# Performance work log

Measured on AMD Instinct MI355X. Metric: run time of the kernel, lower is better.

## Reference

```python
import jax, jax.numpy as jnp
import numpy as np
from jax import lax

A, T, B, OBS, H, ACT = 4, 128, 256, 128, 128, 8  # agents, time, envs, obs_dim, gru_hidden(=embed), act_dim


def setup_inputs() -> dict:
    key = jax.random.key(0)
    ks = jax.random.split(key, 16)
    def w(k, shape, fan_in):
        return (jax.random.normal(k, shape, jnp.float32) / np.float32(np.sqrt(fan_in)))
    return {
        "hstate": jnp.zeros((A, B, H), jnp.float32),
        "obs": jax.random.normal(ks[0], (A, T, B, OBS), jnp.float32),
        "avail_actions": jnp.ones((A, T, B, ACT), jnp.float32),
        # embedding dense
        "We": w(ks[1], (A, OBS, H), OBS), "be": jnp.zeros((A, H), jnp.float32),
        # GRU: input kernels (r|z|n concat) with bias, hidden kernels (r|z|n), only n-hidden has bias
        "Wi": w(ks[2], (A, H, 3 * H), H), "bi": jnp.zeros((A, 3 * H), jnp.float32),
        "Wh": w(ks[3], (A, H, 3 * H), H), "bhn": jnp.zeros((A, H), jnp.float32),
        # actor head
        "Wa1": w(ks[4], (A, H, H), H), "ba1": jnp.zeros((A, H), jnp.float32),
        "Wa2": 0.01 * w(ks[5], (A, H, ACT), H), "ba2": jnp.zeros((A, ACT), jnp.float32),
        "log_std": jnp.zeros((A, ACT), jnp.float32),
        # critic head
        "Wc1": w(ks[6], (A, H, H), H), "bc1": jnp.zeros((A, H), jnp.float32),
        "Wc2": w(ks[7], (A, H, 1), H), "bc2": jnp.zeros((A, 1), jnp.float32),
        "done": jax.random.bernoulli(ks[8], 0.05, (A, T, B)),
    }


def _agent_forward(h0, obs, done, avail_actions, We, be, Wi, bi, Wh, bhn,
                   Wa1, ba1, Wa2, ba2, log_std, Wc1, bc1, Wc2, bc2):
    # obs: [T,B,OBS], done: [T,B], h0: [B,H]
    act = jnp.tanh  # config['network']['activation'] == 'tanh'
    emb = act(jnp.einsum('tbo,oh->tbh', obs, We) + be)          # [T,B,H]
    xi = jnp.einsum('tbh,hg->tbg', emb, Wi) + bi                # [T,B,3H] precomputed input gates

    def step(h, xs):
        xi_t, d = xs                                            # [B,3H], [B]
        h = jnp.where(d[:, None], 0.0, h)                       # reset on done
        hh = h @ Wh                                             # [B,3H]
        xr, xz, xn = jnp.split(xi_t, 3, axis=-1)
        hr, hz, hn = jnp.split(hh, 3, axis=-1)
        r = jax.nn.sigmoid(xr + hr)
        z = jax.nn.sigmoid(xz + hz)
        n = jnp.tanh(xn + r * (hn + bhn))
        h_new = (1.0 - z) * n + z * h
        return h_new, h_new

    hT, ys = lax.scan(step, h0, (xi, done))                     # ys: [T,B,H]
    a = act(jnp.einsum('tbh,hk->tbk', ys, Wa1) + ba1)
    mean = jnp.einsum('tbh,ha->tba', a, Wa2) + ba2              # [T,B,ACT]
    std = jnp.exp(log_std)                                      # [ACT]
    c = act(jnp.einsum('tbh,hk->tbk', ys, Wc1) + bc1)
    value = (jnp.einsum('tbh,ho->tbo', c, Wc2) + bc2)[..., 0]   # [T,B]
    return hT, mean, std, value


def reference(hstate, obs, avail_actions, We, be, Wi, bi, Wh, bhn,
              Wa1, ba1, Wa2, ba2, log_std, Wc1, bc1, Wc2, bc2, done):
    hT, mean, std, value = jax.vmap(_agent_forward)(
        hstate, obs, done, avail_actions, We, be, Wi, bi, Wh, bhn,
        Wa1, ba1, Wa2, ba2, log_std, Wc1, bc1, Wc2, bc2)
    return hT, mean, std, value
```

## Files before the change

kernel.cpp:

```cpp
#include <hip/hip_runtime.h>

typedef unsigned short u16;
typedef __attribute__((ext_vector_type(8))) short short8;
typedef __attribute__((ext_vector_type(4))) float f32x4;

#define A_ 4
#define T_ 128
#define B_ 256
#define OBS_ 128
#define H_ 128
#define G_ 384
#define ACT_ 8

__device__ __forceinline__ u16 f2b(float x) {
    unsigned int u = __float_as_uint(x);
    u = (u + 0x7fffu + ((u >> 16) & 1u)) >> 16;
    return (u16)u;
}
__device__ __forceinline__ u16 f2bc(float x) {
    return (u16)((__float_as_uint(x) + 0x8000u) >> 16);
}
__device__ __forceinline__ float b2f(u16 h) {
    return __uint_as_float(((unsigned int)h) << 16);
}
__device__ __forceinline__ float fexp2_(float x) { return __builtin_amdgcn_exp2f(x); }
__device__ __forceinline__ float frcp_(float x) { return __builtin_amdgcn_rcpf(x); }
__device__ __forceinline__ float sigmoidf_(float x) {
    return frcp_(1.0f + fexp2_(-1.4426950408889634f * x));
}
__device__ __forceinline__ float tanhf_(float x) {
    return 1.0f - 2.0f * frcp_(1.0f + fexp2_(2.8853900817779268f * x));
}
__device__ __forceinline__ f32x4 mfma16(short8 a, short8 b, f32x4 c) {
    return __builtin_amdgcn_mfma_f32_16x16x32_bf16(a, b, c, 0, 0, 0);
}
__device__ __forceinline__ void barrier_fast() {
    asm volatile("s_waitcnt lgkmcnt(0)\n\ts_barrier" ::: "memory");
}

__global__ void k_prep(const float* __restrict__ We, const float* __restrict__ Wi,
                       const float* __restrict__ Wh, const float* __restrict__ Wa1,
                       const float* __restrict__ Wc1, const float* __restrict__ Wa2,
                       const float* __restrict__ Wc2, const float* __restrict__ log_std,
                       u16* __restrict__ weT, u16* __restrict__ wiT, u16* __restrict__ whT,
                       u16* __restrict__ wa1T, u16* __restrict__ wc1T, u16* __restrict__ h2T,
                       float* __restrict__ std_out) {
    const int PER_A = 149504;
    int idx = blockIdx.x * 256 + threadIdx.x;
    const int total = 4 * PER_A;
    if (idx < total) {
        int a = idx / PER_A;
        int i = idx % PER_A;
        if (i < 16384) {
            int h = i >> 7, o = i & 127;
            weT[a * 16384 + i] = f2b(We[a * 16384 + o * 128 + h]);
        } else if (i < 16384 + 49152) {
            int j = i - 16384; int g = j >> 7, k = j & 127;
            wiT[a * 49152 + j] = f2b(Wi[a * 49152 + k * 384 + g]);
        } else if (i < 16384 + 2 * 49152) {
            int j = i - 16384 - 49152; int g = j >> 7, k = j & 127;
            whT[a * 49152 + j] = f2b(Wh[a * 49152 + k * 384 + g]);
        } else if (i < 2 * 16384 + 2 * 49152) {
            int j = i - 16384 - 2 * 49152; int h2 = j >> 7, k = j & 127;
            wa1T[a * 16384 + j] = f2b(Wa1[a * 16384 + k * 128 + h2]);
        } else if (i < 3 * 16384 + 2 * 49152) {
            int j = i - 2 * 16384 - 2 * 49152; int h2 = j >> 7, k = j & 127;
            wc1T[a * 16384 + j] = f2b(Wc1[a * 16384 + k * 128 + h2]);
        } else {
            int j = i - 3 * 16384 - 2 * 49152; int row = j >> 7, k = j & 127;
            float v = 0.f;
            if (row < 8) v = Wa2[a * 1024 + k * 8 + row];
            else if (row == 8) v = Wc2[a * 128 + k];
            h2T[a * 2048 + j] = f2b(v);
        }
    } else if (idx < total + 32) {
        int i = idx - total;
        std_out[i] = __expf(log_std[i]);
    }
}

__global__ __launch_bounds__(512, 2) void k_embed_xi(
    const float* __restrict__ obs, const float* __restrict__ be, const float* __restrict__ bi,
    const u16* __restrict__ weT, const u16* __restrict__ wiT, u16* __restrict__ xi_ws) {
    __shared__ __align__(16) u16 obsl[16][136];
    __shared__ __align__(16) u16 elds[16][136];
    const int a = blockIdx.y, t = blockIdx.x;
    const int wid = threadIdx.x >> 6, lane = threadIdx.x & 63;
    const int m = lane & 15, quad = lane >> 4;
    const int srow = threadIdx.x >> 5, schunk = threadIdx.x & 31;

    short8 we[4], wi[3][4];
    {
        const u16* p = weT + a * 16384 + (wid * 16 + m) * 128 + quad * 8;
#pragma unroll
        for (int ks = 0; ks < 4; ++ks) we[ks] = *(const short8*)(p + ks * 32);
#pragma unroll
        for (int g = 0; g < 3; ++g) {
            const u16* q = wiT + a * 49152 + (g * 128 + wid * 16 + m) * 128 + quad * 8;
#pragma unroll
            for (int ks = 0; ks < 4; ++ks) wi[g][ks] = *(const short8*)(q + ks * 32);
        }
    }
    const float bee = be[a * H_ + wid * 16 + m];
    float big[3];
#pragma unroll
    for (int g = 0; g < 3; ++g) big[g] = bi[a * G_ + g * 128 + wid * 16 + m];

    const float* obsrow = obs + ((size_t)(a * T_ + t) * B_ + srow) * OBS_ + schunk * 4;
    float4 pf = *(const float4*)(obsrow);
    ushort4* xi4 = (ushort4*)xi_ws;

    for (int it = 0; it < 16; ++it) {
        ushort4 ob;
        ob.x = f2b(pf.x); ob.y = f2b(pf.y); ob.z = f2b(pf.z); ob.w = f2b(pf.w);
        *(ushort4*)&obsl[srow][schunk * 4] = ob;
        barrier_fast();
        if (it + 1 < 16) pf = *(const float4*)(obsrow + (size_t)(it + 1) * 2048);

        short8 af[4];
#pragma unroll
        for (int ks = 0; ks < 4; ++ks)
            af[ks] = *(const short8*)&obsl[m][ks * 32 + quad * 8];
        f32x4 acc = f32x4{0.f, 0.f, 0.f, 0.f};
#pragma unroll
        for (int ks = 0; ks < 4; ++ks) acc = mfma16(af[ks], we[ks], acc);
#pragma unroll
        for (int r = 0; r < 4; ++r)
            elds[quad * 4 + r][wid * 16 + m] = f2b(tanhf_(acc[r] + bee));
        barrier_fast();

        short8 ef[4];
#pragma unroll
        for (int ks = 0; ks < 4; ++ks)
            ef[ks] = *(const short8*)&elds[m][ks * 32 + quad * 8];
        f32x4 xa[3];
#pragma unroll
        for (int g = 0; g < 3; ++g) xa[g] = f32x4{0.f, 0.f, 0.f, 0.f};
#pragma unroll
        for (int ks = 0; ks < 4; ++ks)
#pragma unroll
            for (int g = 0; g < 3; ++g) xa[g] = mfma16(ef[ks], wi[g][ks], xa[g]);

        const size_t base = ((size_t)(a * 16 + it) * T_ + t) * 1536;
#pragma unroll
        for (int g = 0; g < 3; ++g) {
            ushort4 pk;
            pk.x = f2b(xa[g][0] + big[g]);
            pk.y = f2b(xa[g][1] + big[g]);
            pk.z = f2b(xa[g][2] + big[g]);
            pk.w = f2b(xa[g][3] + big[g]);
            xi4[base + (size_t)(wid * 3 + g) * 64 + lane] = pk;
        }
    }
}

__global__ __launch_bounds__(512, 2) void k_scan(
    const float* __restrict__ hstate, const u16* __restrict__ xi_ws,
    const u16* __restrict__ whT, const float* __restrict__ bhn,
    const int* __restrict__ done, u16* __restrict__ ys_ws, float* __restrict__ hT_out) {
    __shared__ __align__(16) u16 hlds[2][16][136];
    const int a = blockIdx.y, btile = blockIdx.x;
    const int wid = threadIdx.x >> 6, lane = threadIdx.x & 63;
    const int m = lane & 15, quad = lane >> 4;
    const int b0 = btile * 16;
    const int col = 16 * wid + m;

    short8 wh[3][4];
    const u16* whTa = whT + a * 49152;
#pragma unroll
    for (int g = 0; g < 3; ++g) {
        const u16* p = whTa + (g * 128 + col) * 128 + quad * 8;
#pragma unroll
        for (int ks = 0; ks < 4; ++ks) wh[g][ks] = *(const short8*)(p + ks * 32);
    }

    float hm[4]; u16 hb[4];
#pragma unroll
    for (int r = 0; r < 4; ++r) {
        float v = hstate[((size_t)a * B_ + b0 + quad * 4 + r) * H_ + col];
        hm[r] = v; hb[r] = f2b(v);
    }
    const float bh = bhn[a * H_ + col];

    const ushort4* xi4 = (const ushort4*)xi_ws;
    const size_t xibase = ((size_t)(a * 16 + btile) * T_) * 1536 + wid * 192 + lane;
    const int* dptr = done + (size_t)a * T_ * B_ + b0 + quad * 4;

    ushort4 pA0 = xi4[xibase], pA1 = xi4[xibase + 64], pA2 = xi4[xibase + 128];
    ushort4 pB0 = xi4[xibase + 1536], pB1 = xi4[xibase + 1536 + 64], pB2 = xi4[xibase + 1536 + 128];
    int4 dA = *(const int4*)(dptr);
    int4 dB = *(const int4*)(dptr + B_);

#define SCAN_STEP(t, P0, P1, P2, DN, BUF)                                           \
    {                                                                               \
        u16(*hl)[136] = hlds[BUF];                                                  \
        if (DN.x) { hm[0] = 0.f; hb[0] = 0; }                                       \
        if (DN.y) { hm[1] = 0.f; hb[1] = 0; }                                       \
        if (DN.z) { hm[2] = 0.f; hb[2] = 0; }                                       \
        if (DN.w) { hm[3] = 0.f; hb[3] = 0; }                                       \
        hl[quad * 4 + 0][col] = hb[0];                                              \
        hl[quad * 4 + 1][col] = hb[1];                                              \
        hl[quad * 4 + 2][col] = hb[2];                                              \
        hl[quad * 4 + 3][col] = hb[3];                                              \
        barrier_fast();                                                             \
        float xr[4], xz[4], xn[4];                                                  \
        xr[0] = b2f(P0.x); xr[1] = b2f(P0.y); xr[2] = b2f(P0.z); xr[3] = b2f(P0.w); \
        xz[0] = b2f(P1.x); xz[1] = b2f(P1.y); xz[2] = b2f(P1.z); xz[3] = b2f(P1.w); \
        xn[0] = b2f(P2.x); xn[1] = b2f(P2.y); xn[2] = b2f(P2.z); xn[3] = b2f(P2.w); \
        if ((t) + 2 < T_) {                                                         \
            const size_t nx = xibase + (size_t)((t) + 2) * 1536;                    \
            P0 = xi4[nx]; P1 = xi4[nx + 64]; P2 = xi4[nx + 128];                    \
            DN = *(const int4*)(dptr + (size_t)((t) + 2) * B_);                     \
        }                                                                           \
        short8 af[4];                                                               \
        af[0] = *(const short8*)&hl[m][0 * 32 + quad * 8];                          \
        af[1] = *(const short8*)&hl[m][1 * 32 + quad * 8];                          \
        af[2] = *(const short8*)&hl[m][2 * 32 + quad * 8];                          \
        af[3] = *(const short8*)&hl[m][3 * 32 + quad * 8];                          \
        f32x4 ar = f32x4{0.f, 0.f, 0.f, 0.f};                                       \
        f32x4 az = f32x4{0.f, 0.f, 0.f, 0.f};                                       \
        f32x4 an = f32x4{0.f, 0.f, 0.f, 0.f};                                       \
        _Pragma("unroll") for (int ks = 0; ks < 4; ++ks) {                          \
            ar = mfma16(af[ks], wh[0][ks], ar);                                     \
            az = mfma16(af[ks], wh[1][ks], az);                                     \
            an = mfma16(af[ks], wh[2][ks], an);                                     \
        }                                                                           \
        u16* yp = ys_ws + (((size_t)a * T_ + (t)) * B_ + b0 + quad * 4) * H_ + col; \
        _Pragma("unroll") for (int r = 0; r < 4; ++r) {                             \
            const float rg = sigmoidf_(xr[r] + ar[r]);                              \
            const float zg = sigmoidf_(xz[r] + az[r]);                              \
            const float ng = tanhf_(fmaf(rg, an[r] + bh, xn[r]));                   \
            const float hn2 = fmaf(zg, hm[r] - ng, ng);                             \
            hm[r] = hn2;                                                            \
            hb[r] = f2bc(hn2);                                                      \
            yp[(size_t)r * H_] = hb[r];                                             \
        }                                                                           \
    }

    for (int t = 0; t < T_; t += 2) {
        SCAN_STEP(t, pA0, pA1, pA2, dA, 0);
        SCAN_STEP(t + 1, pB0, pB1, pB2, dB, 1);
    }
#undef SCAN_STEP

#pragma unroll
    for (int r = 0; r < 4; ++r)
        hT_out[((size_t)a * B_ + b0 + quad * 4 + r) * H_ + col] = hm[r];
}

__global__ __launch_bounds__(512, 2) void k_heads(
    const u16* __restrict__ ys_ws, const u16* __restrict__ wa1T, const u16* __restrict__ wc1T,
    const u16* __restrict__ h2T, const float* __restrict__ ba1, const float* __restrict__ bc1,
    const float* __restrict__ ba2, const float* __restrict__ bc2,
    float* __restrict__ mean_out, float* __restrict__ val_out) {
    __shared__ __align__(16) u16 ysl[16][136];
    __shared__ __align__(16) u16 al[2][16][136];
    const int a = blockIdx.y;
    const int wid = threadIdx.x >> 6, lane = threadIdx.x & 63;
    const int m = lane & 15, quad = lane >> 4;
    const int srow = threadIdx.x >> 5, schunk = threadIdx.x & 31;

    short8 wa[4], wc[4], h2f[4];
    {
        const u16* pa = wa1T + a * 16384 + (wid * 16 + m) * 128 + quad * 8;
        const u16* pc = wc1T + a * 16384 + (wid * 16 + m) * 128 + quad * 8;
        const u16* ph = h2T + a * 2048 + m * 128 + quad * 8;
#pragma unroll
        for (int ks = 0; ks < 4; ++ks) {
            wa[ks] = *(const short8*)(pa + ks * 32);
            wc[ks] = *(const short8*)(pc + ks * 32);
            h2f[ks] = *(const short8*)(ph + ks * 32);
        }
    }
    const float fa = ba1[a * 128 + wid * 16 + m];
    const float fc = bc1[a * 128 + wid * 16 + m];

    const u16* ysbase = ys_ws + ((size_t)a * 32768 + (size_t)blockIdx.x * 256 + srow) * 128 + schunk * 4;
    ushort4 pf = *(const ushort4*)(ysbase);

    for (int it = 0; it < 16; ++it) {
        *(ushort4*)&ysl[srow][schunk * 4] = pf;
        barrier_fast();
        if (it + 1 < 16) pf = *(const ushort4*)(ysbase + (size_t)(it + 1) * 2048);

        short8 yf[4];
#pragma unroll
        for (int ks = 0; ks < 4; ++ks)
            yf[ks] = *(const short8*)&ysl[m][ks * 32 + quad * 8];
        f32x4 aa = f32x4{0.f, 0.f, 0.f, 0.f};
        f32x4 ac = f32x4{0.f, 0.f, 0.f, 0.f};
#pragma unroll
        for (int ks = 0; ks < 4; ++ks) {
            aa = mfma16(yf[ks], wa[ks], aa);
            ac = mfma16(yf[ks], wc[ks], ac);
        }
#pragma unroll
        for (int r = 0; r < 4; ++r) {
            al[0][quad * 4 + r][wid * 16 + m] = f2b(tanhf_(aa[r] + fa));
            al[1][quad * 4 + r][wid * 16 + m] = f2b(tanhf_(ac[r] + fc));
        }
        barrier_fast();

        if (wid < 2) {
            short8 tf[4];
#pragma unroll
            for (int ks = 0; ks < 4; ++ks)
                tf[ks] = *(const short8*)&al[wid][m][ks * 32 + quad * 8];
            f32x4 tacc = f32x4{0.f, 0.f, 0.f, 0.f};
#pragma unroll
            for (int ks = 0; ks < 4; ++ks) tacc = mfma16(tf[ks], h2f[ks], tacc);
            const size_t R0 = (size_t)a * 32768 + (size_t)(blockIdx.x * 16 + it) * 16;
            if (wid == 0) {
                if (m < 8) {
                    const float bb = ba2[a * 8 + m];
#pragma unroll
                    for (int r = 0; r < 4; ++r)
                        mean_out[(R0 + quad * 4 + r) * 8 + m] = tacc[r] + bb;
                }
            } else {
                if (m == 8) {
                    const float bb = bc2[a];
#pragma unroll
                    for (int r = 0; r < 4; ++r)
                        val_out[R0 + quad * 4 + r] = tacc[r] + bb;
                }
            }
        }
    }
}

extern "C" void kernel_launch(void* const* d_in, const int* in_sizes, int n_in,
                              void* d_out, int out_size, void* d_ws, size_t ws_size,
                              hipStream_t stream) {
    const float* hstate = (const float*)d_in[0];
    const float* obs = (const float*)d_in[1];
    const float* We = (const float*)d_in[3];
    const float* be = (const float*)d_in[4];
    const float* Wi = (const float*)d_in[5];
    const float* bi = (const float*)d_in[6];
    const float* Wh = (const float*)d_in[7];
    const float* bhn = (const float*)d_in[8];
    const float* Wa1 = (const float*)d_in[9];
    const float* ba1 = (const float*)d_in[10];
    const float* Wa2 = (const float*)d_in[11];
    const float* ba2 = (const float*)d_in[12];
    const float* log_std = (const float*)d_in[13];
    const float* Wc1 = (const float*)d_in[14];
    const float* bc1 = (const float*)d_in[15];
    const float* Wc2 = (const float*)d_in[16];
    const float* bc2 = (const float*)d_in[17];
    const int* done = (const int*)d_in[18];

    float* out = (float*)d_out;
    float* hT_out = out;
    float* mean_out = out + 131072;
    float* std_out = out + 1179648;
    float* val_out = out + 1179680;

    u16* ws = (u16*)d_ws;
    u16* xi = ws;
    u16* ys = xi + 50331648;
    u16* weT = ys + 16777216;
    u16* wiT = weT + 65536;
    u16* whT = wiT + 196608;
    u16* wa1T = whT + 196608;
    u16* wc1T = wa1T + 65536;
    u16* h2T = wc1T + 65536;

    hipLaunchKernelGGL(k_prep, dim3(2337), dim3(256), 0, stream,
                       We, Wi, Wh, Wa1, Wc1, Wa2, Wc2, log_std,
                       weT, wiT, whT, wa1T, wc1T, h2T, std_out);
    hipLaunchKernelGGL(k_embed_xi, dim3(128, 4), dim3(512), 0, stream,
                       obs, be, bi, weT, wiT, xi);
    hipLaunchKernelGGL(k_scan, dim3(16, 4), dim3(512), 0, stream,
                       hstate, xi, whT, bhn, done, ys, hT_out);
    hipLaunchKernelGGL(k_heads, dim3(128, 4), dim3(512), 0, stream,
                       ys, wa1T, wc1T, h2T, ba1, bc1, ba2, bc2, mean_out, val_out);
}
```

Before: 312.2 us.

## Pack two batch tiles per scan block and strength-reduce scan pointers

The GRU scan kernel now runs 1024-thread blocks, each covering two 16-row batch tiles, so the grid is half as many blocks, each with its own pair of LDS hidden-state buffers. Per-step address computation for the xi, done and ys streams becomes pointer increments instead of recomputed offsets. Launch bounds are raised on both the scan and heads kernels to request higher occupancy. The risks are that each step's barrier now spans sixteen waves, and that the tighter launch bounds may force register spills in the weight-resident scan and head kernels.

```diff
diff --git a/kernel.cpp b/kernel.cpp
--- a/kernel.cpp
+++ b/kernel.cpp
@@ -154,16 +154,19 @@
     }
 }
 
-__global__ __launch_bounds__(512, 2) void k_scan(
+__global__ __launch_bounds__(1024, 4) void k_scan(
     const float* __restrict__ hstate, const u16* __restrict__ xi_ws,
     const u16* __restrict__ whT, const float* __restrict__ bhn,
     const int* __restrict__ done, u16* __restrict__ ys_ws, float* __restrict__ hT_out) {
-    __shared__ __align__(16) u16 hlds[2][16][136];
-    const int a = blockIdx.y, btile = blockIdx.x;
+    __shared__ __align__(16) u16 hlds[2][2][16][136];
+    const int a = blockIdx.y;
     const int wid = threadIdx.x >> 6, lane = threadIdx.x & 63;
+    const int bl = wid >> 3;
+    const int wq = wid & 7;
+    const int btile = blockIdx.x * 2 + bl;
     const int m = lane & 15, quad = lane >> 4;
     const int b0 = btile * 16;
-    const int col = 16 * wid + m;
+    const int col = 16 * wq + m;
 
     short8 wh[3][4];
     const u16* whTa = whT + a * 49152;
@@ -183,7 +186,7 @@
     const float bh = bhn[a * H_ + col];
 
     const ushort4* xi4 = (const ushort4*)xi_ws;
-    const size_t xibase = ((size_t)(a * 16 + btile) * T_) * 1536 + wid * 192 + lane;
+    const size_t xibase = ((size_t)(a * 16 + btile) * T_) * 1536 + wq * 192 + lane;
     const int* dptr = done + (size_t)a * T_ * B_ + b0 + quad * 4;
 
     ushort4 pA0 = xi4[xibase], pA1 = xi4[xibase + 64], pA2 = xi4[xibase + 128];
@@ -191,9 +194,16 @@
     int4 dA = *(const int4*)(dptr);
     int4 dB = *(const int4*)(dptr + B_);
 
-#define SCAN_STEP(t, P0, P1, P2, DN, BUF)                                           \
+    const ushort4* xpA = xi4 + xibase + 2 * 1536;
+    const ushort4* xpB = xi4 + xibase + 3 * 1536;
+    const int* dpA = dptr + 2 * B_;
+    const int* dpB = dptr + 3 * B_;
+    u16* ypA = ys_ws + ((size_t)a * T_ * B_ + b0 + quad * 4) * H_ + col;
+    u16* ypB = ypA + (size_t)B_ * H_;
+
+#define SCAN_STEP(t, P0, P1, P2, DN, XP, DP, YP, BUF)                               \
     {                                                                               \
-        u16(*hl)[136] = hlds[BUF];                                                  \
+        u16(*hl)[136] = hlds[bl][BUF];                                              \
         if (DN.x) { hm[0] = 0.f; hb[0] = 0; }                                       \
         if (DN.y) { hm[1] = 0.f; hb[1] = 0; }                                       \
         if (DN.z) { hm[2] = 0.f; hb[2] = 0; }                                       \
@@ -208,10 +218,10 @@
         xz[0] = b2f(P1.x); xz[1] = b2f(P1.y); xz[2] = b2f(P1.z); xz[3] = b2f(P1.w); \
         xn[0] = b2f(P2.x); xn[1] = b2f(P2.y); xn[2] = b2f(P2.z); xn[3] = b2f(P2.w); \
         if ((t) + 2 < T_) {                                                         \
-            const size_t nx = xibase + (size_t)((t) + 2) * 1536;                    \
-            P0 = xi4[nx]; P1 = xi4[nx + 64]; P2 = xi4[nx + 128];                    \
-            DN = *(const int4*)(dptr + (size_t)((t) + 2) * B_);                     \
+            P0 = XP[0]; P1 = XP[64]; P2 = XP[128];                                  \
+            DN = *(const int4*)(DP);                                                \
         }                                                                           \
+        XP += 3072; DP += 2 * B_;                                                   \
         short8 af[4];                                                               \
         af[0] = *(const short8*)&hl[m][0 * 32 + quad * 8];                          \
         af[1] = *(const short8*)&hl[m][1 * 32 + quad * 8];                          \
@@ -225,7 +235,6 @@
             az = mfma16(af[ks], wh[1][ks], az);                                     \
             an = mfma16(af[ks], wh[2][ks], an);                                     \
         }                                                                           \
-        u16* yp = ys_ws + (((size_t)a * T_ + (t)) * B_ + b0 + quad * 4) * H_ + col; \
         _Pragma("unroll") for (int r = 0; r < 4; ++r) {                             \
             const float rg = sigmoidf_(xr[r] + ar[r]);                              \
             const float zg = sigmoidf_(xz[r] + az[r]);                              \
@@ -233,13 +242,14 @@
             const float hn2 = fmaf(zg, hm[r] - ng, ng);                             \
             hm[r] = hn2;                                                            \
             hb[r] = f2bc(hn2);                                                      \
-            yp[(size_t)r * H_] = hb[r];                                             \
+            YP[(size_t)r * H_] = hb[r];                                             \
         }                                                                           \
+        YP += 2 * B_ * H_;                                                          \
     }
 
     for (int t = 0; t < T_; t += 2) {
-        SCAN_STEP(t, pA0, pA1, pA2, dA, 0);
-        SCAN_STEP(t + 1, pB0, pB1, pB2, dB, 1);
+        SCAN_STEP(t, pA0, pA1, pA2, dA, xpA, dpA, ypA, 0);
+        SCAN_STEP(t + 1, pB0, pB1, pB2, dB, xpB, dpB, ypB, 1);
     }
 #undef SCAN_STEP
 
@@ -248,7 +258,7 @@
         hT_out[((size_t)a * B_ + b0 + quad * 4 + r) * H_ + col] = hm[r];
 }
 
-__global__ __launch_bounds__(512, 2) void k_heads(
+__global__ __launch_bounds__(512, 4) void k_heads(
     const u16* __restrict__ ys_ws, const u16* __restrict__ wa1T, const u16* __restrict__ wc1T,
     const u16* __restrict__ h2T, const float* __restrict__ ba1, const float* __restrict__ bc1,
     const float* __restrict__ ba2, const float* __restrict__ bc2,
@@ -372,7 +382,7 @@
                        weT, wiT, whT, wa1T, wc1T, h2T, std_out);
     hipLaunchKernelGGL(k_embed_xi, dim3(128, 4), dim3(512), 0, stream,
                        obs, be, bi, weT, wiT, xi);
-    hipLaunchKernelGGL(k_scan, dim3(16, 4), dim3(512), 0, stream,
+    hipLaunchKernelGGL(k_scan, dim3(8, 4), dim3(1024), 0, stream,
                        hstate, xi, whT, bhn, done, ys, hT_out);
     hipLaunchKernelGGL(k_heads, dim3(128, 4), dim3(512), 0, stream,
                        ys, wa1T, wc1T, h2T, ba1, bc1, ba2, bc2, mean_out, val_out);
```

Measured after the change: 383.8 us. 1.23x slower.
